# Performance work log

Measured on AMD Instinct MI355X. Metric: run time of the kernel, lower is better.

The kernel has to match this reference:

```python
import jax, jax.numpy as jnp
import numpy as np

P, B, S = 128, 32, 64          # num_packet, batch, bytes per packet
E = 50                          # byte/packet embedding size (hard-coded in module)
Hb = 128; Hp = 128; Po = 128   # byte hidden, packet hidden, packet output
V = 256 * 256; NCLS = 11


def setup_inputs() -> dict:
    key = jax.random.key(0)
    ks = jax.random.split(key, 12)
    rn = lambda k, shp, s: (jax.random.normal(k, shp, jnp.float32) * s)
    return {
        'flow': jax.random.randint(ks[0], (P, B, S), 0, V),
        'emb': rn(ks[1], (V, E), 0.1),
        'byte_Wih': rn(ks[2], (2, 3 * Hb, E), 1.0 / np.sqrt(E)),
        'byte_Whh': rn(ks[3], (2, 3 * Hb, Hb), 1.0 / np.sqrt(Hb)),
        'byte_attn_W': rn(ks[4], (E, 2 * Hb), 1.0 / np.sqrt(2 * Hb)),
        'byte_attn_b': jnp.zeros((E,), jnp.float32),
        'pkt_Wih': rn(ks[5], (2, 3 * Hp, E), 1.0 / np.sqrt(E)),
        'pkt_Whh': rn(ks[6], (2, 3 * Hp, Hp), 1.0 / np.sqrt(Hp)),
        'pkt_attn_W': rn(ks[7], (Po, 2 * Hp), 1.0 / np.sqrt(2 * Hp)),
        'pkt_attn_b': jnp.zeros((Po,), jnp.float32),
        'cls_W': rn(ks[8], (NCLS, Po), 1.0 / np.sqrt(Po)),
        'cls_b': jnp.zeros((NCLS,), jnp.float32),
        'h0_bytes': rn(ks[9], (P, 2, B, Hb), 1.0),   # per-packet random h0 (torch.randn in fwd)
        'h0_packet': rn(ks[10], (2, B, Hp), 1.0),
    }


def _gru_dir(xW, h0, Whh, H):
    # xW: (S, N, 3H) precomputed input projections; h0: (N, H). PyTorch gate order r,z,n; no bias.
    def step(h, xw):
        hW = h @ Whh.T
        r = jax.nn.sigmoid(xw[:, :H] + hW[:, :H])
        z = jax.nn.sigmoid(xw[:, H:2 * H] + hW[:, H:2 * H])
        n = jnp.tanh(xw[:, 2 * H:] + r * hW[:, 2 * H:])
        h_new = (1.0 - z) * n + z * h
        return h_new, h_new
    hT, ys = jax.lax.scan(step, h0, xW)
    return ys, hT


def bigru(x, h0, Wih, Whh, H):
    # x: (S, N, E); h0: (2, N, H) -> outputs (S, N, 2H), final hidden (2, N, H)
    xWf = jnp.einsum('sne,ge->sng', x, Wih[0])
    xWb = jnp.einsum('sne,ge->sng', x[::-1], Wih[1])
    yf, hf = _gru_dir(xWf, h0[0], Whh[0], H)
    yb, hb = _gru_dir(xWb, h0[1], Whh[1], H)
    return jnp.concatenate([yf, yb[::-1]], axis=-1), jnp.stack([hf, hb])


def reference(flow, emb, byte_Wih, byte_Whh, byte_attn_W, byte_attn_b,
              pkt_Wih, pkt_Whh, pkt_attn_W, pkt_attn_b, cls_W, cls_b,
              h0_bytes, h0_packet):
    Pn, Bn, Sn = flow.shape
    x = emb[flow]                                             # (P, B, S, E)
    # Fold packets into batch: one byte-level bi-GRU call instead of a Python loop over P.
    xs = x.transpose(2, 0, 1, 3).reshape(Sn, Pn * Bn, E)      # (S, P*B, E)
    h0b = h0_bytes.transpose(1, 0, 2, 3).reshape(2, Pn * Bn, Hb)
    y, hn = bigru(xs, h0b, byte_Wih, byte_Whh, Hb)            # y (S, P*B, 2Hb), hn (2, P*B, Hb)
    out = y.transpose(1, 0, 2).reshape(Pn, Bn, Sn, 2 * Hb)    # (P, B, S, 2Hb)
    # torch view(-1, 2Hb, 1) on each per-packet (2, B, Hb) final state == raw C-order reshape
    hn_p = hn.reshape(2, Pn, Bn, Hb).transpose(1, 0, 2, 3).reshape(Pn, Bn, 2 * Hb)
    aw = jax.nn.softmax(jnp.einsum('pbsh,pbh->pbs', out, hn_p), axis=-1)
    ctx = jnp.einsum('pbsh,pbs->pbh', out, aw)                # (P, B, 2Hb)
    enc = ctx @ byte_attn_W.T + byte_attn_b                   # (P, B, E)

    y2, hn2 = bigru(enc, h0_packet, pkt_Wih, pkt_Whh, Hp)     # (P, B, 2Hp), (2, B, Hp)
    out2 = y2.transpose(1, 0, 2)                              # (B, P, 2Hp)
    hn2v = hn2.reshape(Bn, 2 * Hp)                            # view(-1, byte_hidden*2) semantics
    aw2 = jax.nn.softmax(jnp.einsum('bph,bh->bp', out2, hn2v), axis=-1)
    ctx2 = jnp.einsum('bph,bp->bh', out2, aw2)                # (B, 2Hp)
    o = ctx2 @ pkt_attn_W.T + pkt_attn_b                      # (B, Po)
    return o @ cls_W.T + cls_b                                # (B, 11)
```

## Files before the change

kernel.cpp:

```cpp
#include <hip/hip_runtime.h>
#include <hip/hip_bf16.h>

#define PD 128
#define BD 32
#define SD 64
#define ED 50
#define EP 52
#define HD 128
#define GD 384
#define ND 4096
#define VD 65536

typedef __attribute__((ext_vector_type(8))) short bf16x8;
typedef __attribute__((ext_vector_type(4))) float f32x4;

__device__ __forceinline__ float sigm(float x) { return 1.0f / (1.0f + __expf(-x)); }
__device__ __forceinline__ float tanh_f(float x) { return 1.0f - 2.0f / (__expf(2.0f * x) + 1.0f); }

__device__ __forceinline__ unsigned short f2b(float f) {
    union { float f; unsigned u; } a; a.f = f;
    unsigned r = a.u + 0x7FFFu + ((a.u >> 16) & 1u);
    return (unsigned short)(r >> 16);
}
__device__ __forceinline__ float b2f(unsigned short h) {
    union { unsigned u; float f; } a; a.u = ((unsigned)h) << 16; return a.f;
}

union frag_u { bf16x8 v; unsigned short s[8]; };

__device__ __forceinline__ void pin_v(bf16x8& v) { asm volatile("" : "+v"(v)); }
__device__ __forceinline__ void pin_a(bf16x8& v) { asm volatile("" : "+a"(v)); }

#define MFMA(acc, a, b) acc = __builtin_amdgcn_mfma_f32_16x16x32_bf16(a, b, acc, 0, 0, 0)

__device__ __forceinline__ void block_sync_lds() {
    asm volatile("s_waitcnt lgkmcnt(0)" ::: "memory");
    __builtin_amdgcn_sched_barrier(0);
    __builtin_amdgcn_s_barrier();
    __builtin_amdgcn_sched_barrier(0);
}

__global__ void prep_emb(const float* __restrict__ emb, unsigned short* __restrict__ embHi) {
    int idx = blockIdx.x * 256 + threadIdx.x;
    if (idx >= VD * 64) return;
    int row = idx >> 6, e = idx & 63;
    float v = (e < ED) ? emb[row * ED + e] : 0.f;
    embHi[idx] = f2b(v);
}

__global__ void prep_pad_pkt(const float* __restrict__ pw, float* __restrict__ pP) {
    int idx = blockIdx.x * 256 + threadIdx.x;
    if (idx >= 2 * GD * EP) return;
    int row = idx / EP, e = idx - row * EP;
    pP[idx] = (e < ED) ? pw[row * ED + e] : 0.f;
}

__global__ __attribute__((amdgpu_flat_work_group_size(512, 512), amdgpu_waves_per_eu(2, 2)))
void byte_gru_mfma(
    const int* __restrict__ flow, const unsigned short* __restrict__ embHi,
    const float* __restrict__ Wih, const float* __restrict__ Whh,
    const float* __restrict__ h0b,
    unsigned short* __restrict__ y, float* __restrict__ hn) {
    const int dir   = blockIdx.x >> 7;
    const int chunk = blockIdx.x & 127;
    const int n0    = chunk * 32;
    const int tid   = threadIdx.x;
    const int w     = tid >> 6;
    const int lane  = tid & 63;
    const int col   = lane & 15;
    const int kq    = lane >> 4;
    const int u     = w * 16 + col;

    __shared__ unsigned short HHI[2][32 * 128];
    __shared__ unsigned short HLO[2][32 * 128];
    __shared__ int FLOWT[SD * 32];

    bf16x8 WHh[3][4], WHl[3][4], WXh[3][2], WXl[3][2];
    {
        const float* WhhD = Whh + dir * GD * HD;
        #pragma unroll
        for (int g3 = 0; g3 < 3; ++g3) {
            const float* row = WhhD + (g3 * HD + u) * HD;
            #pragma unroll
            for (int kt = 0; kt < 4; ++kt) {
                const int k0 = kt * 32 + kq * 8;
                frag_u h_, l_;
                #pragma unroll
                for (int b = 0; b < 8; ++b) {
                    float v = row[k0 + b];
                    unsigned short hi = f2b(v);
                    h_.s[b] = hi; l_.s[b] = f2b(v - b2f(hi));
                }
                WHh[g3][kt] = h_.v; WHl[g3][kt] = l_.v;
            }
        }
        const float* WihD = Wih + dir * GD * ED;
        #pragma unroll
        for (int g3 = 0; g3 < 3; ++g3) {
            const float* row = WihD + (g3 * HD + u) * ED;
            #pragma unroll
            for (int kx = 0; kx < 2; ++kx) {
                const int k0 = kx * 32 + kq * 8;
                frag_u h_, l_;
                #pragma unroll
                for (int b = 0; b < 8; ++b) {
                    const int e = k0 + b;
                    float v = (e < ED) ? row[e] : 0.f;
                    unsigned short hi = f2b(v);
                    h_.s[b] = hi; l_.s[b] = f2b(v - b2f(hi));
                }
                WXh[g3][kx] = h_.v; WXl[g3][kx] = l_.v;
            }
        }
    }

    float hreg[2][4];
    {
        const float* h0row = h0b + (size_t)((chunk * 2 + dir) * 32) * HD;
        #pragma unroll
        for (int m = 0; m < 2; ++m)
            #pragma unroll
            for (int j = 0; j < 4; ++j)
                hreg[m][j] = h0row[(m * 16 + kq * 4 + j) * HD + u];
        for (int idx = tid; idx < 32 * HD; idx += 512) {
            int seq = idx >> 7, uu = idx & 127;
            float v = h0row[idx];
            unsigned short hi = f2b(v);
            int sw = seq * 128 + (uu ^ ((seq & 7) << 3));
            HHI[0][sw] = hi; HLO[0][sw] = f2b(v - b2f(hi));
        }
        for (int j = tid; j < SD * 32; j += 512) {
            int s = j >> 5, seq = j & 31;
            FLOWT[j] = flow[(n0 + seq) * SD + s];
        }
    }
    block_sync_lds();

    int par = 0;
    for (int t = 0; t < SD; ++t) {
        const int s = dir ? (SD - 1 - t) : t;

        bf16x8 xa00, xa01, xa10, xa11;
        {
            int i0 = FLOWT[s * 32 + col];
            int i1 = FLOWT[s * 32 + 16 + col];
            const bf16x8* r0 = (const bf16x8*)(embHi + (size_t)i0 * 64);
            const bf16x8* r1 = (const bf16x8*)(embHi + (size_t)i1 * 64);
            xa00 = r0[kq]; xa01 = r0[4 + kq];
            xa10 = r1[kq]; xa11 = r1[4 + kq];
        }

        f32x4 aR[2], aZ[2], aHN[2], aXN[2];
        const f32x4 zero = {0.f, 0.f, 0.f, 0.f};
        #pragma unroll
        for (int m = 0; m < 2; ++m) { aR[m] = zero; aZ[m] = zero; aHN[m] = zero; aXN[m] = zero; }

        const unsigned short* HHIp = HHI[par];
        const unsigned short* HLOp = HLO[par];
        #pragma unroll
        for (int kt = 0; kt < 4; ++kt) {
            const int off = kt * 32 + kq * 8;
            const int sw0 = col * 128 + (off ^ ((col & 7) << 3));
            const int sw1 = sw0 + 16 * 128;
            bf16x8 ah0 = *(const bf16x8*)&HHIp[sw0];
            bf16x8 al0 = *(const bf16x8*)&HLOp[sw0];
            bf16x8 ah1 = *(const bf16x8*)&HHIp[sw1];
            bf16x8 al1 = *(const bf16x8*)&HLOp[sw1];
            MFMA(aR[0], ah0, WHh[0][kt]); MFMA(aR[0], al0, WHh[0][kt]); MFMA(aR[0], ah0, WHl[0][kt]);
            MFMA(aZ[0], ah0, WHh[1][kt]); MFMA(aZ[0], al0, WHh[1][kt]); MFMA(aZ[0], ah0, WHl[1][kt]);
            MFMA(aHN[0], ah0, WHh[2][kt]); MFMA(aHN[0], al0, WHh[2][kt]); MFMA(aHN[0], ah0, WHl[2][kt]);
            MFMA(aR[1], ah1, WHh[0][kt]); MFMA(aR[1], al1, WHh[0][kt]); MFMA(aR[1], ah1, WHl[0][kt]);
            MFMA(aZ[1], ah1, WHh[1][kt]); MFMA(aZ[1], al1, WHh[1][kt]); MFMA(aZ[1], ah1, WHl[1][kt]);
            MFMA(aHN[1], ah1, WHh[2][kt]); MFMA(aHN[1], al1, WHh[2][kt]); MFMA(aHN[1], ah1, WHl[2][kt]);
        }
        #pragma unroll
        for (int kx = 0; kx < 2; ++kx) {
            bf16x8 x0 = kx ? xa01 : xa00;
            bf16x8 x1 = kx ? xa11 : xa10;
            MFMA(aR[0], x0, WXh[0][kx]); MFMA(aR[0], x0, WXl[0][kx]);
            MFMA(aZ[0], x0, WXh[1][kx]); MFMA(aZ[0], x0, WXl[1][kx]);
            MFMA(aXN[0], x0, WXh[2][kx]); MFMA(aXN[0], x0, WXl[2][kx]);
            MFMA(aR[1], x1, WXh[0][kx]); MFMA(aR[1], x1, WXl[0][kx]);
            MFMA(aZ[1], x1, WXh[1][kx]); MFMA(aZ[1], x1, WXl[1][kx]);
            MFMA(aXN[1], x1, WXh[2][kx]); MFMA(aXN[1], x1, WXl[2][kx]);
        }

        unsigned short* HHIn = HHI[par ^ 1];
        unsigned short* HLOn = HLO[par ^ 1];
        #pragma unroll
        for (int m = 0; m < 2; ++m)
            #pragma unroll
            for (int j = 0; j < 4; ++j) {
                float r = sigm(aR[m][j]);
                float z = sigm(aZ[m][j]);
                float nn = tanh_f(aXN[m][j] + r * aHN[m][j]);
                float hnew = (1.f - z) * nn + z * hreg[m][j];
                hreg[m][j] = hnew;
                __hip_bfloat16 bh = __float2bfloat16(hnew);
                unsigned short hi = *(unsigned short*)&bh;
                __hip_bfloat16 bl = __float2bfloat16(hnew - b2f(hi));
                unsigned short lo = *(unsigned short*)&bl;
                const int seq = m * 16 + kq * 4 + j;
                const int sw = seq * 128 + (u ^ ((seq & 7) << 3));
                HHIn[sw] = hi;
                HLOn[sw] = lo;
                y[((size_t)(s * ND) + n0 + seq) * 256 + dir * HD + u] = hi;
            }
        block_sync_lds();
        #pragma unroll
        for (int g3 = 0; g3 < 3; ++g3) {
            #pragma unroll
            for (int kt = 0; kt < 4; ++kt) { pin_v(WHh[g3][kt]); pin_a(WHl[g3][kt]); }
            #pragma unroll
            for (int kx = 0; kx < 2; ++kx) { pin_a(WXh[g3][kx]); pin_a(WXl[g3][kx]); }
        }
        par ^= 1;
    }
    #pragma unroll
    for (int m = 0; m < 2; ++m)
        #pragma unroll
        for (int j = 0; j < 4; ++j) {
            int seq = m * 16 + kq * 4 + j;
            hn[((size_t)dir * ND + n0 + seq) * HD + u] = hreg[m][j];
        }
}

__global__ __launch_bounds__(256) void byte_attn(
    const unsigned short* __restrict__ y, const float* __restrict__ hn,
    const float* __restrict__ aW, const float* __restrict__ ab,
    float* __restrict__ enc) {
    const int n = blockIdx.x;
    const int p = n >> 5, irow = n & 31;
    const int tid = threadIdx.x;
    __shared__ unsigned short yl[SD][256];
    __shared__ float hnl[256];
    __shared__ float red[256];
    __shared__ float awl[SD];
    __shared__ float ctxl[256];

    for (int idx = tid; idx < SD * 32; idx += 256) {
        int s = idx >> 5, cc = (idx & 31) * 8;
        *(uint4*)&yl[s][cc] = *(const uint4*)&y[((s * ND) + n) * 256 + cc];
    }
    {
        int c = tid;
        int idx = irow * 256 + c;
        int d = idx >> 12, bb = (idx >> 7) & 31, uu = idx & 127;
        hnl[c] = hn[(d * ND + p * 32 + bb) * HD + uu];
    }
    __syncthreads();
    {
        int s = tid & 63, grp = tid >> 6;
        float acc = 0.f;
        for (int k = 0; k < 32; ++k) {
            int c2 = grp * 32 + ((s + k) & 31);
            unsigned pair = *(const unsigned*)&yl[s][c2 * 2];
            float2 hv = *(const float2*)&hnl[c2 * 2];
            union { unsigned u; float f; } lo, hi;
            lo.u = pair << 16; hi.u = pair & 0xFFFF0000u;
            acc += lo.f * hv.x + hi.f * hv.y;
        }
        red[grp * 64 + s] = acc;
    }
    __syncthreads();
    if (tid < 64) {
        float sc = red[tid] + red[64 + tid] + red[128 + tid] + red[192 + tid];
        float m = sc;
        #pragma unroll
        for (int o = 32; o; o >>= 1) m = fmaxf(m, __shfl_xor(m, o));
        float e = __expf(sc - m);
        float ssum = e;
        #pragma unroll
        for (int o = 32; o; o >>= 1) ssum += __shfl_xor(ssum, o);
        awl[tid] = e / ssum;
    }
    __syncthreads();
    {
        int c = tid;
        float acc = 0.f;
        for (int s = 0; s < SD; ++s) acc += awl[s] * b2f(yl[s][c]);
        ctxl[c] = acc;
    }
    __syncthreads();
    {
        int e = tid & 63, q = tid >> 6;
        float acc = 0.f;
        if (e < ED) {
            for (int c = q * 64; c < q * 64 + 64; ++c) acc += ctxl[c] * aW[e * 256 + c];
        }
        red[q * 64 + e] = acc;
    }
    __syncthreads();
    if (tid < EP) {
        float v = 0.f;
        if (tid < ED) v = red[tid] + red[64 + tid] + red[128 + tid] + red[192 + tid] + ab[tid];
        enc[n * EP + tid] = v;
    }
}

__global__ __launch_bounds__(256, 1) void pkt_xw(
    const float* __restrict__ enc, const float* __restrict__ WihPp,
    float* __restrict__ pxw) {
    const int d = blockIdx.x >> 7, p = blockIdx.x & 127;
    const int tid = threadIdx.x;
    __shared__ float el[32][EP];
    for (int idx = tid; idx < 32 * EP; idx += 256) {
        int ii = idx / EP, e = idx - ii * EP;
        el[ii][e] = enc[(p * 32 + ii) * EP + e];
    }
    __syncthreads();
    const int irow = tid & 31, gg = tid >> 5;
    const float* W = WihPp + d * GD * EP;
    float acc[48];
    #pragma unroll
    for (int j = 0; j < 48; ++j) acc[j] = 0.f;
    for (int ec = 0; ec < 13; ++ec) {
        float4 x4 = *(const float4*)&el[irow][ec * 4];
        #pragma unroll
        for (int j = 0; j < 48; ++j) {
            float4 w4 = *(const float4*)(W + (gg + 8 * j) * EP + ec * 4);
            acc[j] += x4.x * w4.x + x4.y * w4.y + x4.z * w4.z + x4.w * w4.w;
        }
    }
    float* dst = pxw + (size_t)((d * PD + p) * 32 + irow) * GD;
    #pragma unroll
    for (int j = 0; j < 48; ++j) dst[gg + 8 * j] = acc[j];
}

__global__ __launch_bounds__(384, 1) void pkt_gru(
    const float* __restrict__ pxw, const float* __restrict__ Whh,
    const float* __restrict__ h0p,
    float* __restrict__ y2, float* __restrict__ hn2) {
    const int d = blockIdx.x >> 5, sq = blockIdx.x & 31;
    const int tid = threadIdx.x;
    __shared__ float hcur[HD];
    __shared__ float hw[GD];
    float w[HD];
    const float* wrow = Whh + (d * GD + tid) * HD;
    #pragma unroll
    for (int k = 0; k < HD; ++k) w[k] = wrow[k];
    if (tid < HD) hcur[tid] = h0p[(d * 32 + sq) * HD + tid];

    float xr = 0.f, xz = 0.f, xn_ = 0.f;
    if (tid < HD) {
        const int p0 = d ? (PD - 1) : 0;
        const float* xw = pxw + (size_t)((d * PD + p0) * 32 + sq) * GD;
        xr = xw[tid]; xz = xw[HD + tid]; xn_ = xw[2 * HD + tid];
    }
    block_sync_lds();
    for (int t = 0; t < PD; ++t) {
        const int pp = d ? (PD - 1 - t) : t;
        float xrn = 0.f, xzn = 0.f, xnn = 0.f;
        if (t < PD - 1 && tid < HD) {
            const int pn = d ? (PD - 2 - t) : (t + 1);
            const float* xw = pxw + (size_t)((d * PD + pn) * 32 + sq) * GD;
            xrn = xw[tid]; xzn = xw[HD + tid]; xnn = xw[2 * HD + tid];
        }
        float a0 = 0.f, a1 = 0.f, a2 = 0.f, a3 = 0.f;
        #pragma unroll
        for (int kc = 0; kc < 32; ++kc) {
            float4 h4 = *(const float4*)&hcur[kc * 4];
            a0 += w[4 * kc + 0] * h4.x; a1 += w[4 * kc + 1] * h4.y;
            a2 += w[4 * kc + 2] * h4.z; a3 += w[4 * kc + 3] * h4.w;
        }
        hw[tid] = (a0 + a1) + (a2 + a3);
        block_sync_lds();
        if (tid < HD) {
            int uu = tid;
            float r = sigm(xr + hw[uu]);
            float z = sigm(xz + hw[HD + uu]);
            float nn = tanh_f(xn_ + r * hw[2 * HD + uu]);
            float hnew = (1.f - z) * nn + z * hcur[uu];
            hcur[uu] = hnew;
            y2[(pp * 32 + sq) * 256 + d * HD + uu] = hnew;
        }
        block_sync_lds();
        xr = xrn; xz = xzn; xn_ = xnn;
    }
    if (tid < HD) hn2[(d * 32 + sq) * HD + tid] = hcur[tid];
}

__global__ __launch_bounds__(256) void pkt_attn_cls(
    const float* __restrict__ y2, const float* __restrict__ hn2,
    const float* __restrict__ aW, const float* __restrict__ ab,
    const float* __restrict__ cW, const float* __restrict__ cb,
    float* __restrict__ out) {
    const int b = blockIdx.x;
    const int tid = threadIdx.x;
    __shared__ float hnl[256];
    __shared__ float red[256];
    __shared__ float scl[PD];
    __shared__ float awl[PD];
    __shared__ float ctxl[256];
    __shared__ float ol[HD];
    {
        int c = tid;
        hnl[c] = hn2[(((b >> 4) * 32) + 2 * (b & 15) + (c >> 7)) * HD + (c & 127)];
    }
    __syncthreads();
    {
        int p2 = tid >> 1, hf = tid & 1;
        const float* yr = y2 + (p2 * 32 + b) * 256 + hf * 128;
        const float* hr = hnl + hf * 128;
        float acc = 0.f;
        for (int c = 0; c < 128; ++c) acc += yr[c] * hr[c];
        red[hf * 128 + p2] = acc;
    }
    __syncthreads();
    if (tid < PD) scl[tid] = red[tid] + red[128 + tid];
    __syncthreads();
    if (tid < 64) {
        float s0 = scl[tid], s1 = scl[64 + tid];
        float m = fmaxf(s0, s1);
        #pragma unroll
        for (int o = 32; o; o >>= 1) m = fmaxf(m, __shfl_xor(m, o));
        float e0 = __expf(s0 - m), e1 = __expf(s1 - m);
        float ss = e0 + e1;
        #pragma unroll
        for (int o = 32; o; o >>= 1) ss += __shfl_xor(ss, o);
        awl[tid] = e0 / ss; awl[64 + tid] = e1 / ss;
    }
    __syncthreads();
    {
        int c = tid;
        float acc = 0.f;
        for (int p2 = 0; p2 < PD; ++p2) acc += awl[p2] * y2[(p2 * 32 + b) * 256 + c];
        ctxl[c] = acc;
    }
    __syncthreads();
    {
        int h = tid >> 1, hf = tid & 1;
        const float* wr = aW + h * 256 + hf * 128;
        const float* cr = ctxl + hf * 128;
        float acc = 0.f;
        for (int c = 0; c < 128; ++c) acc += cr[c] * wr[c];
        red[hf * 128 + h] = acc;
    }
    __syncthreads();
    if (tid < HD) ol[tid] = red[tid] + red[128 + tid] + ab[tid];
    __syncthreads();
    if (tid < 11) {
        float acc = cb[tid];
        for (int h = 0; h < HD; ++h) acc += ol[h] * cW[tid * HD + h];
        out[b * 11 + tid] = acc;
    }
}

extern "C" void kernel_launch(void* const* d_in, const int* in_sizes, int n_in,
                              void* d_out, int out_size, void* d_ws, size_t ws_size,
                              hipStream_t stream) {
    const int*   flow = (const int*)d_in[0];
    const float* emb  = (const float*)d_in[1];
    const float* bWih = (const float*)d_in[2];
    const float* bWhh = (const float*)d_in[3];
    const float* baW  = (const float*)d_in[4];
    const float* bab  = (const float*)d_in[5];
    const float* pWih = (const float*)d_in[6];
    const float* pWhh = (const float*)d_in[7];
    const float* paW  = (const float*)d_in[8];
    const float* pab  = (const float*)d_in[9];
    const float* cW   = (const float*)d_in[10];
    const float* cb   = (const float*)d_in[11];
    const float* h0b  = (const float*)d_in[12];
    const float* h0p  = (const float*)d_in[13];
    float* out = (float*)d_out;

    char* ws = (char*)d_ws;
    size_t off = 0;
    unsigned short* y = (unsigned short*)(ws + off); off += (size_t)SD * ND * 256 * 2;
    float* hn    = (float*)(ws + off); off += (size_t)2 * ND * HD * 4;
    float* enc   = (float*)(ws + off); off += (size_t)ND * EP * 4;
    float* pxw   = (float*)(ws + off); off += (size_t)2 * PD * 32 * GD * 4;
    float* y2    = (float*)(ws + off); off += (size_t)PD * 32 * 256 * 4;
    float* hn2   = (float*)(ws + off); off += (size_t)2 * 32 * HD * 4;
    float* WihPp = (float*)(ws + off); off += (size_t)2 * GD * EP * 4;
    unsigned short* embHi = (unsigned short*)(ws + off); off += (size_t)VD * 64 * 2;
    if (ws_size < off) return;

    prep_emb<<<(VD * 64 + 255) / 256, 256, 0, stream>>>(emb, embHi);
    prep_pad_pkt<<<(2 * GD * EP + 255) / 256, 256, 0, stream>>>(pWih, WihPp);
    byte_gru_mfma<<<256, 512, 0, stream>>>(flow, embHi, bWih, bWhh, h0b, y, hn);
    byte_attn<<<ND, 256, 0, stream>>>(y, hn, baW, bab, enc);
    pkt_xw<<<256, 256, 0, stream>>>(enc, WihPp, pxw);
    pkt_gru<<<64, 384, 0, stream>>>(pxw, pWhh, h0p, y2, hn2);
    pkt_attn_cls<<<32, 256, 0, stream>>>(y2, hn2, paW, pab, cW, cb, out);
}
```

Measured before the change: 552.0 us.

## Drop low-part input-weight MFMAs, pad LDS rows, fuse prep kernels

Stops splitting the input-projection weights into hi/lo bf16 parts, which removes half of the x-side MFMAs in the byte GRU step. The embedding input is already a single bf16, so the extra precision was of limited value, but accuracy of the input projection drops slightly. It also pads the LDS hidden-state rows to 132 elements to change the bank mapping, moves the register pinning from every step to load time (keeping weights in VGPRs rather than AGPRs), and merges the two prep kernels into a single launch.

```diff
diff --git a/kernel.cpp b/kernel.cpp
--- a/kernel.cpp
+++ b/kernel.cpp
@@ -10,6 +10,7 @@
 #define GD 384
 #define ND 4096
 #define VD 65536
+#define LW 132
 
 typedef __attribute__((ext_vector_type(8))) short bf16x8;
 typedef __attribute__((ext_vector_type(4))) float f32x4;
@@ -29,7 +30,6 @@
 union frag_u { bf16x8 v; unsigned short s[8]; };
 
 __device__ __forceinline__ void pin_v(bf16x8& v) { asm volatile("" : "+v"(v)); }
-__device__ __forceinline__ void pin_a(bf16x8& v) { asm volatile("" : "+a"(v)); }
 
 #define MFMA(acc, a, b) acc = __builtin_amdgcn_mfma_f32_16x16x32_bf16(a, b, acc, 0, 0, 0)
 
@@ -40,19 +40,18 @@
     __builtin_amdgcn_sched_barrier(0);
 }
 
-__global__ void prep_emb(const float* __restrict__ emb, unsigned short* __restrict__ embHi) {
+__global__ void prep_all(const float* __restrict__ emb, unsigned short* __restrict__ embHi,
+                         const float* __restrict__ pw, float* __restrict__ pP) {
     int idx = blockIdx.x * 256 + threadIdx.x;
-    if (idx >= VD * 64) return;
-    int row = idx >> 6, e = idx & 63;
-    float v = (e < ED) ? emb[row * ED + e] : 0.f;
-    embHi[idx] = f2b(v);
-}
-
-__global__ void prep_pad_pkt(const float* __restrict__ pw, float* __restrict__ pP) {
-    int idx = blockIdx.x * 256 + threadIdx.x;
-    if (idx >= 2 * GD * EP) return;
-    int row = idx / EP, e = idx - row * EP;
-    pP[idx] = (e < ED) ? pw[row * ED + e] : 0.f;
+    if (idx < VD * 64) {
+        int row = idx >> 6, e = idx & 63;
+        float v = (e < ED) ? emb[row * ED + e] : 0.f;
+        embHi[idx] = f2b(v);
+    }
+    if (idx < 2 * GD * EP) {
+        int row = idx / EP, e = idx - row * EP;
+        pP[idx] = (e < ED) ? pw[row * ED + e] : 0.f;
+    }
 }
 
 __global__ __attribute__((amdgpu_flat_work_group_size(512, 512), amdgpu_waves_per_eu(2, 2)))
@@ -71,11 +70,11 @@
     const int kq    = lane >> 4;
     const int u     = w * 16 + col;
 
-    __shared__ unsigned short HHI[2][32 * 128];
-    __shared__ unsigned short HLO[2][32 * 128];
+    __shared__ unsigned short HHI[2][32 * LW];
+    __shared__ unsigned short HLO[2][32 * LW];
     __shared__ int FLOWT[SD * 32];
 
-    bf16x8 WHh[3][4], WHl[3][4], WXh[3][2], WXl[3][2];
+    bf16x8 WHh[3][4], WHl[3][4], WXh[3][2];
     {
         const float* WhhD = Whh + dir * GD * HD;
         #pragma unroll
@@ -92,6 +91,7 @@
                     h_.s[b] = hi; l_.s[b] = f2b(v - b2f(hi));
                 }
                 WHh[g3][kt] = h_.v; WHl[g3][kt] = l_.v;
+                pin_v(WHh[g3][kt]); pin_v(WHl[g3][kt]);
             }
         }
         const float* WihD = Wih + dir * GD * ED;
@@ -101,15 +101,15 @@
             #pragma unroll
             for (int kx = 0; kx < 2; ++kx) {
                 const int k0 = kx * 32 + kq * 8;
-                frag_u h_, l_;
+                frag_u h_;
                 #pragma unroll
                 for (int b = 0; b < 8; ++b) {
                     const int e = k0 + b;
                     float v = (e < ED) ? row[e] : 0.f;
-                    unsigned short hi = f2b(v);
-                    h_.s[b] = hi; l_.s[b] = f2b(v - b2f(hi));
+                    h_.s[b] = f2b(v);
                 }
-                WXh[g3][kx] = h_.v; WXl[g3][kx] = l_.v;
+                WXh[g3][kx] = h_.v;
+                pin_v(WXh[g3][kx]);
             }
         }
     }
@@ -126,7 +126,7 @@
             int seq = idx >> 7, uu = idx & 127;
             float v = h0row[idx];
             unsigned short hi = f2b(v);
-            int sw = seq * 128 + (uu ^ ((seq & 7) << 3));
+            int sw = seq * LW + (uu ^ ((seq & 7) << 3));
             HHI[0][sw] = hi; HLO[0][sw] = f2b(v - b2f(hi));
         }
         for (int j = tid; j < SD * 32; j += 512) {
@@ -160,8 +160,8 @@
         #pragma unroll
         for (int kt = 0; kt < 4; ++kt) {
             const int off = kt * 32 + kq * 8;
-            const int sw0 = col * 128 + (off ^ ((col & 7) << 3));
-            const int sw1 = sw0 + 16 * 128;
+            const int sw0 = col * LW + (off ^ ((col & 7) << 3));
+            const int sw1 = sw0 + 16 * LW;
             bf16x8 ah0 = *(const bf16x8*)&HHIp[sw0];
             bf16x8 al0 = *(const bf16x8*)&HLOp[sw0];
             bf16x8 ah1 = *(const bf16x8*)&HHIp[sw1];
@@ -177,12 +177,12 @@
         for (int kx = 0; kx < 2; ++kx) {
             bf16x8 x0 = kx ? xa01 : xa00;
             bf16x8 x1 = kx ? xa11 : xa10;
-            MFMA(aR[0], x0, WXh[0][kx]); MFMA(aR[0], x0, WXl[0][kx]);
-            MFMA(aZ[0], x0, WXh[1][kx]); MFMA(aZ[0], x0, WXl[1][kx]);
-            MFMA(aXN[0], x0, WXh[2][kx]); MFMA(aXN[0], x0, WXl[2][kx]);
-            MFMA(aR[1], x1, WXh[0][kx]); MFMA(aR[1], x1, WXl[0][kx]);
-            MFMA(aZ[1], x1, WXh[1][kx]); MFMA(aZ[1], x1, WXl[1][kx]);
-            MFMA(aXN[1], x1, WXh[2][kx]); MFMA(aXN[1], x1, WXl[2][kx]);
+            MFMA(aR[0], x0, WXh[0][kx]);
+            MFMA(aZ[0], x0, WXh[1][kx]);
+            MFMA(aXN[0], x0, WXh[2][kx]);
+            MFMA(aR[1], x1, WXh[0][kx]);
+            MFMA(aZ[1], x1, WXh[1][kx]);
+            MFMA(aXN[1], x1, WXh[2][kx]);
         }
 
         unsigned short* HHIn = HHI[par ^ 1];
@@ -201,19 +201,12 @@
                 __hip_bfloat16 bl = __float2bfloat16(hnew - b2f(hi));
                 unsigned short lo = *(unsigned short*)&bl;
                 const int seq = m * 16 + kq * 4 + j;
-                const int sw = seq * 128 + (u ^ ((seq & 7) << 3));
+                const int sw = seq * LW + (u ^ ((seq & 7) << 3));
                 HHIn[sw] = hi;
                 HLOn[sw] = lo;
                 y[((size_t)(s * ND) + n0 + seq) * 256 + dir * HD + u] = hi;
             }
         block_sync_lds();
-        #pragma unroll
-        for (int g3 = 0; g3 < 3; ++g3) {
-            #pragma unroll
-            for (int kt = 0; kt < 4; ++kt) { pin_v(WHh[g3][kt]); pin_a(WHl[g3][kt]); }
-            #pragma unroll
-            for (int kx = 0; kx < 2; ++kx) { pin_a(WXh[g3][kx]); pin_a(WXl[g3][kx]); }
-        }
         par ^= 1;
     }
     #pragma unroll
@@ -477,8 +470,7 @@
     unsigned short* embHi = (unsigned short*)(ws + off); off += (size_t)VD * 64 * 2;
     if (ws_size < off) return;
 
-    prep_emb<<<(VD * 64 + 255) / 256, 256, 0, stream>>>(emb, embHi);
-    prep_pad_pkt<<<(2 * GD * EP + 255) / 256, 256, 0, stream>>>(pWih, WihPp);
+    prep_all<<<(VD * 64 + 255) / 256, 256, 0, stream>>>(emb, embHi, pWih, WihPp);
     byte_gru_mfma<<<256, 512, 0, stream>>>(flow, embHi, bWih, bWhh, h0b, y, hn);
     byte_attn<<<ND, 256, 0, stream>>>(y, hn, baW, bab, enc);
     pkt_xw<<<256, 256, 0, stream>>>(enc, WihPp, pxw);
```

After: 698.8 us. 26.6% more time.

## Prefetch embeddings, coalesce y stores, fuse packet input projection into byte attention

Applied to the files above, without the earlier changes.

In the byte GRU, the next step's embedding rows are now prefetched during the current step. The per-element y stores are replaced by 16-byte vector stores read back from the shared-memory h buffer after the barrier. The packet-GRU input projection (pkt_xw) and the padded-weight prep kernel are folded into byte_attn, which removes two launches and the enc round trip through global memory. The packet attention-score pass now stages y2 rows in shared memory so loads are coalesced. Register pinning of the weight fragments also changes from AGPR to VGPR, which may raise register pressure in the recurrent loop.

```diff
diff --git a/kernel.cpp b/kernel.cpp
--- a/kernel.cpp
+++ b/kernel.cpp
@@ -10,6 +10,7 @@
 #define GD 384
 #define ND 4096
 #define VD 65536
+#define LW 128
 
 typedef __attribute__((ext_vector_type(8))) short bf16x8;
 typedef __attribute__((ext_vector_type(4))) float f32x4;
@@ -29,7 +30,6 @@
 union frag_u { bf16x8 v; unsigned short s[8]; };
 
 __device__ __forceinline__ void pin_v(bf16x8& v) { asm volatile("" : "+v"(v)); }
-__device__ __forceinline__ void pin_a(bf16x8& v) { asm volatile("" : "+a"(v)); }
 
 #define MFMA(acc, a, b) acc = __builtin_amdgcn_mfma_f32_16x16x32_bf16(a, b, acc, 0, 0, 0)
 
@@ -46,13 +46,6 @@
     int row = idx >> 6, e = idx & 63;
     float v = (e < ED) ? emb[row * ED + e] : 0.f;
     embHi[idx] = f2b(v);
-}
-
-__global__ void prep_pad_pkt(const float* __restrict__ pw, float* __restrict__ pP) {
-    int idx = blockIdx.x * 256 + threadIdx.x;
-    if (idx >= 2 * GD * EP) return;
-    int row = idx / EP, e = idx - row * EP;
-    pP[idx] = (e < ED) ? pw[row * ED + e] : 0.f;
 }
 
 __global__ __attribute__((amdgpu_flat_work_group_size(512, 512), amdgpu_waves_per_eu(2, 2)))
@@ -71,9 +64,13 @@
     const int kq    = lane >> 4;
     const int u     = w * 16 + col;
 
-    __shared__ unsigned short HHI[2][32 * 128];
-    __shared__ unsigned short HLO[2][32 * 128];
+    __shared__ unsigned short HHI[2][32 * LW];
+    __shared__ unsigned short HLO[2][32 * LW];
     __shared__ int FLOWT[SD * 32];
+
+    const int yrow = tid >> 4;
+    const int yu0  = (tid & 15) * 8;
+    const int ysw  = yrow * LW + (yu0 ^ ((yrow & 7) << 3));
 
     bf16x8 WHh[3][4], WHl[3][4], WXh[3][2], WXl[3][2];
     {
@@ -92,6 +89,7 @@
                     h_.s[b] = hi; l_.s[b] = f2b(v - b2f(hi));
                 }
                 WHh[g3][kt] = h_.v; WHl[g3][kt] = l_.v;
+                pin_v(WHh[g3][kt]); pin_v(WHl[g3][kt]);
             }
         }
         const float* WihD = Wih + dir * GD * ED;
@@ -110,6 +108,7 @@
                     h_.s[b] = hi; l_.s[b] = f2b(v - b2f(hi));
                 }
                 WXh[g3][kx] = h_.v; WXl[g3][kx] = l_.v;
+                pin_v(WXh[g3][kx]); pin_v(WXl[g3][kx]);
             }
         }
     }
@@ -126,7 +125,7 @@
             int seq = idx >> 7, uu = idx & 127;
             float v = h0row[idx];
             unsigned short hi = f2b(v);
-            int sw = seq * 128 + (uu ^ ((seq & 7) << 3));
+            int sw = seq * LW + (uu ^ ((seq & 7) << 3));
             HHI[0][sw] = hi; HLO[0][sw] = f2b(v - b2f(hi));
         }
         for (int j = tid; j < SD * 32; j += 512) {
@@ -136,18 +135,36 @@
     }
     block_sync_lds();
 
+    bf16x8 xa00, xa01, xa10, xa11;
+    {
+        const int s0 = dir ? (SD - 1) : 0;
+        int i0 = FLOWT[s0 * 32 + col];
+        int i1 = FLOWT[s0 * 32 + 16 + col];
+        const bf16x8* r0 = (const bf16x8*)(embHi + (size_t)i0 * 64);
+        const bf16x8* r1 = (const bf16x8*)(embHi + (size_t)i1 * 64);
+        xa00 = r0[kq]; xa01 = r0[4 + kq];
+        xa10 = r1[kq]; xa11 = r1[4 + kq];
+    }
+
     int par = 0;
     for (int t = 0; t < SD; ++t) {
         const int s = dir ? (SD - 1 - t) : t;
 
-        bf16x8 xa00, xa01, xa10, xa11;
-        {
-            int i0 = FLOWT[s * 32 + col];
-            int i1 = FLOWT[s * 32 + 16 + col];
+        if (t > 0) {
+            const int sp = dir ? (SD - t) : (t - 1);
+            uint4 v = *(const uint4*)&HHI[par][ysw];
+            *(uint4*)&y[((size_t)(sp * ND) + n0 + yrow) * 256 + dir * HD + yu0] = v;
+        }
+
+        bf16x8 xn00, xn01, xn10, xn11;
+        if (t < SD - 1) {
+            const int sn = dir ? (SD - 2 - t) : (t + 1);
+            int i0 = FLOWT[sn * 32 + col];
+            int i1 = FLOWT[sn * 32 + 16 + col];
             const bf16x8* r0 = (const bf16x8*)(embHi + (size_t)i0 * 64);
             const bf16x8* r1 = (const bf16x8*)(embHi + (size_t)i1 * 64);
-            xa00 = r0[kq]; xa01 = r0[4 + kq];
-            xa10 = r1[kq]; xa11 = r1[4 + kq];
+            xn00 = r0[kq]; xn01 = r0[4 + kq];
+            xn10 = r1[kq]; xn11 = r1[4 + kq];
         }
 
         f32x4 aR[2], aZ[2], aHN[2], aXN[2];
@@ -160,8 +177,8 @@
         #pragma unroll
         for (int kt = 0; kt < 4; ++kt) {
             const int off = kt * 32 + kq * 8;
-            const int sw0 = col * 128 + (off ^ ((col & 7) << 3));
-            const int sw1 = sw0 + 16 * 128;
+            const int sw0 = col * LW + (off ^ ((col & 7) << 3));
+            const int sw1 = sw0 + 16 * LW;
             bf16x8 ah0 = *(const bf16x8*)&HHIp[sw0];
             bf16x8 al0 = *(const bf16x8*)&HLOp[sw0];
             bf16x8 ah1 = *(const bf16x8*)&HHIp[sw1];
@@ -199,22 +216,19 @@
                 __hip_bfloat16 bh = __float2bfloat16(hnew);
                 unsigned short hi = *(unsigned short*)&bh;
                 __hip_bfloat16 bl = __float2bfloat16(hnew - b2f(hi));
-                unsigned short lo = *(unsigned short*)&bl;
                 const int seq = m * 16 + kq * 4 + j;
-                const int sw = seq * 128 + (u ^ ((seq & 7) << 3));
+                const int sw = seq * LW + (u ^ ((seq & 7) << 3));
                 HHIn[sw] = hi;
-                HLOn[sw] = lo;
-                y[((size_t)(s * ND) + n0 + seq) * 256 + dir * HD + u] = hi;
+                HLOn[sw] = *(unsigned short*)&bl;
             }
         block_sync_lds();
-        #pragma unroll
-        for (int g3 = 0; g3 < 3; ++g3) {
-            #pragma unroll
-            for (int kt = 0; kt < 4; ++kt) { pin_v(WHh[g3][kt]); pin_a(WHl[g3][kt]); }
-            #pragma unroll
-            for (int kx = 0; kx < 2; ++kx) { pin_a(WXh[g3][kx]); pin_a(WXl[g3][kx]); }
-        }
+        xa00 = xn00; xa01 = xn01; xa10 = xn10; xa11 = xn11;
         par ^= 1;
+    }
+    {
+        const int sl = dir ? 0 : (SD - 1);
+        uint4 v = *(const uint4*)&HHI[par][ysw];
+        *(uint4*)&y[((size_t)(sl * ND) + n0 + yrow) * 256 + dir * HD + yu0] = v;
     }
     #pragma unroll
     for (int m = 0; m < 2; ++m)
@@ -228,7 +242,7 @@
 __global__ __launch_bounds__(256) void byte_attn(
     const unsigned short* __restrict__ y, const float* __restrict__ hn,
     const float* __restrict__ aW, const float* __restrict__ ab,
-    float* __restrict__ enc) {
+    const float* __restrict__ pWih, float* __restrict__ pxw) {
     const int n = blockIdx.x;
     const int p = n >> 5, irow = n & 31;
     const int tid = threadIdx.x;
@@ -237,6 +251,7 @@
     __shared__ float red[256];
     __shared__ float awl[SD];
     __shared__ float ctxl[256];
+    __shared__ float encl[ED];
 
     for (int idx = tid; idx < SD * 32; idx += 256) {
         int s = idx >> 5, cc = (idx & 31) * 8;
@@ -291,40 +306,17 @@
         red[q * 64 + e] = acc;
     }
     __syncthreads();
-    if (tid < EP) {
-        float v = 0.f;
-        if (tid < ED) v = red[tid] + red[64 + tid] + red[128 + tid] + red[192 + tid] + ab[tid];
-        enc[n * EP + tid] = v;
-    }
-}
-
-__global__ __launch_bounds__(256, 1) void pkt_xw(
-    const float* __restrict__ enc, const float* __restrict__ WihPp,
-    float* __restrict__ pxw) {
-    const int d = blockIdx.x >> 7, p = blockIdx.x & 127;
-    const int tid = threadIdx.x;
-    __shared__ float el[32][EP];
-    for (int idx = tid; idx < 32 * EP; idx += 256) {
-        int ii = idx / EP, e = idx - ii * EP;
-        el[ii][e] = enc[(p * 32 + ii) * EP + e];
-    }
-    __syncthreads();
-    const int irow = tid & 31, gg = tid >> 5;
-    const float* W = WihPp + d * GD * EP;
-    float acc[48];
+    if (tid < ED) encl[tid] = red[tid] + red[64 + tid] + red[128 + tid] + red[192 + tid] + ab[tid];
+    __syncthreads();
     #pragma unroll
-    for (int j = 0; j < 48; ++j) acc[j] = 0.f;
-    for (int ec = 0; ec < 13; ++ec) {
-        float4 x4 = *(const float4*)&el[irow][ec * 4];
-        #pragma unroll
-        for (int j = 0; j < 48; ++j) {
-            float4 w4 = *(const float4*)(W + (gg + 8 * j) * EP + ec * 4);
-            acc[j] += x4.x * w4.x + x4.y * w4.y + x4.z * w4.z + x4.w * w4.w;
-        }
-    }
-    float* dst = pxw + (size_t)((d * PD + p) * 32 + irow) * GD;
-    #pragma unroll
-    for (int j = 0; j < 48; ++j) dst[gg + 8 * j] = acc[j];
+    for (int k = 0; k < 3; ++k) {
+        int fg = tid + k * 256;
+        int d = fg >= GD, g = fg - d * GD;
+        const float* wr = pWih + (size_t)(d * GD + g) * ED;
+        float acc = 0.f;
+        for (int e = 0; e < ED; ++e) acc += encl[e] * wr[e];
+        pxw[((size_t)(d * PD + p) * 32 + irow) * GD + g] = acc;
+    }
 }
 
 __global__ __launch_bounds__(384, 1) void pkt_gru(
@@ -387,27 +379,38 @@
     float* __restrict__ out) {
     const int b = blockIdx.x;
     const int tid = threadIdx.x;
+    __shared__ float yl2[32][257];
     __shared__ float hnl[256];
     __shared__ float red[256];
     __shared__ float scl[PD];
     __shared__ float awl[PD];
     __shared__ float ctxl[256];
     __shared__ float ol[HD];
-    {
-        int c = tid;
-        hnl[c] = hn2[(((b >> 4) * 32) + 2 * (b & 15) + (c >> 7)) * HD + (c & 127)];
-    }
-    __syncthreads();
-    {
-        int p2 = tid >> 1, hf = tid & 1;
-        const float* yr = y2 + (p2 * 32 + b) * 256 + hf * 128;
-        const float* hr = hnl + hf * 128;
-        float acc = 0.f;
-        for (int c = 0; c < 128; ++c) acc += yr[c] * hr[c];
-        red[hf * 128 + p2] = acc;
-    }
-    __syncthreads();
-    if (tid < PD) scl[tid] = red[tid] + red[128 + tid];
+    hnl[tid] = hn2[(((b >> 4) * 32) + 2 * (b & 15) + (tid >> 7)) * HD + (tid & 127)];
+    for (int ch = 0; ch < 4; ++ch) {
+        __syncthreads();
+        for (int idx = tid; idx < 32 * 256; idx += 256) {
+            int r = idx >> 8, c = idx & 255;
+            yl2[r][c] = y2[((ch * 32 + r) * 32 + b) * 256 + c];
+        }
+        __syncthreads();
+        {
+            int r = tid >> 3, seg = tid & 7;
+            float acc = 0.f;
+            for (int i = 0; i < 32; ++i) {
+                int c = seg * 32 + ((i + seg * 4) & 31);
+                acc += yl2[r][c] * hnl[c];
+            }
+            red[tid] = acc;
+        }
+        __syncthreads();
+        if (tid < 32) {
+            float s = 0.f;
+            #pragma unroll
+            for (int k = 0; k < 8; ++k) s += red[tid * 8 + k];
+            scl[ch * 32 + tid] = s;
+        }
+    }
     __syncthreads();
     if (tid < 64) {
         float s0 = scl[tid], s1 = scl[64 + tid];
@@ -469,19 +472,15 @@
     size_t off = 0;
     unsigned short* y = (unsigned short*)(ws + off); off += (size_t)SD * ND * 256 * 2;
     float* hn    = (float*)(ws + off); off += (size_t)2 * ND * HD * 4;
-    float* enc   = (float*)(ws + off); off += (size_t)ND * EP * 4;
     float* pxw   = (float*)(ws + off); off += (size_t)2 * PD * 32 * GD * 4;
     float* y2    = (float*)(ws + off); off += (size_t)PD * 32 * 256 * 4;
     float* hn2   = (float*)(ws + off); off += (size_t)2 * 32 * HD * 4;
-    float* WihPp = (float*)(ws + off); off += (size_t)2 * GD * EP * 4;
     unsigned short* embHi = (unsigned short*)(ws + off); off += (size_t)VD * 64 * 2;
     if (ws_size < off) return;
 
     prep_emb<<<(VD * 64 + 255) / 256, 256, 0, stream>>>(emb, embHi);
-    prep_pad_pkt<<<(2 * GD * EP + 255) / 256, 256, 0, stream>>>(pWih, WihPp);
     byte_gru_mfma<<<256, 512, 0, stream>>>(flow, embHi, bWih, bWhh, h0b, y, hn);
-    byte_attn<<<ND, 256, 0, stream>>>(y, hn, baW, bab, enc);
-    pkt_xw<<<256, 256, 0, stream>>>(enc, WihPp, pxw);
+    byte_attn<<<ND, 256, 0, stream>>>(y, hn, baW, bab, pWih, pxw);
     pkt_gru<<<64, 384, 0, stream>>>(pxw, pWhh, h0p, y2, hn2);
     pkt_attn_cls<<<32, 256, 0, stream>>>(y2, hn2, paW, pab, cW, cb, out);
 }
```

Result: no change. 554.6 us (+0.5%).
